# Kernel tuning notes

Measured on AMD Instinct MI355X. Metric: run time of the kernel, lower is better.

The kernel has to match this reference:

```python
import jax, jax.numpy as jnp
import numpy as np

K = 20
EPS = 1e-5
DIMS = [(8, 64), (64, 64), (64, 128), (128, 256), (256, 512), (512, 1024)]
EMB = 512


def edge_conv(x, W, gamma, beta):
    # x: [B, C, N]; W: [O, 2C]
    xt = jnp.swapaxes(x, 1, 2)                      # [B, N, C]
    inner = -2.0 * jnp.einsum('bnc,bmc->bnm', xt, xt)
    xx = jnp.sum(xt * xt, axis=-1)                  # [B, N]
    pd = -xx[:, :, None] - inner - xx[:, None, :]   # -||xi-xj||^2
    idx = jax.lax.top_k(pd, K)[1]                   # [B, N, K]
    nbr = jax.vmap(lambda f, i: f[i])(xt, idx)      # [B, N, K, C] gather
    ctr = xt[:, :, None, :]
    edge = jnp.concatenate([nbr - ctr, jnp.broadcast_to(ctr, nbr.shape)], axis=-1)  # [B,N,K,2C]
    h = jnp.einsum('bnkc,oc->bnko', edge, W)        # 1x1 conv
    mean = jnp.mean(h, axis=(0, 1, 2))
    var = jnp.var(h, axis=(0, 1, 2))
    h = (h - mean) * jax.lax.rsqrt(var + EPS) * gamma + beta  # BatchNorm2d (train stats)
    h = jnp.where(h > 0, h, 0.2 * h)                # LeakyReLU(0.2)
    return jnp.transpose(jnp.max(h, axis=2), (0, 2, 1))  # max over k -> [B, O, N]


def setup_inputs() -> dict:
    key = jax.random.key(0)
    ks = jax.random.split(key, 32)
    d = {"x": jax.random.normal(ks[0], (4, 8, 1024), dtype=jnp.float32)}
    for i, (cin, cout) in enumerate(DIMS):
        fan_in = 2 * cin
        std = float(np.sqrt(2.0 / ((1.0 + 0.2 ** 2) * fan_in)))
        d[f"W{i+1}"] = jax.random.normal(ks[1 + i], (cout, 2 * cin), dtype=jnp.float32) * std
        d[f"g{i+1}"] = jnp.ones((cout,), dtype=jnp.float32)
        d[f"b{i+1}"] = jnp.zeros((cout,), dtype=jnp.float32)
    d["Wm"] = jax.random.normal(ks[20], (EMB, 4096), dtype=jnp.float32) * float(1.0 / np.sqrt(4096))
    d["bm"] = jnp.zeros((EMB,), dtype=jnp.float32)
    d["gm"] = jnp.ones((EMB,), dtype=jnp.float32)
    d["betam"] = jnp.zeros((EMB,), dtype=jnp.float32)
    return d


def reference(x, W1, g1, b1, W2, g2, b2, W3, g3, b3, W4, g4, b4,
              W5, g5, b5, W6, g6, b6, Wm, bm, gm, betam):
    x1 = edge_conv(x, W1, g1, b1)
    x2 = edge_conv(x1, W2, g2, b2)
    x3 = edge_conv(x2, W3, g3, b3)
    x4 = edge_conv(x3, W4, g4, b4)
    x5 = edge_conv(x4, W5, g5, b5)
    x6 = edge_conv(x5, W6, g6, b6)
    feat = jnp.concatenate([x1, x2, x3, x4, x5, x6], axis=1)  # [B, 2048, N]
    p1 = jnp.max(feat, axis=-1)
    p2 = jnp.mean(feat, axis=-1)
    z = jnp.concatenate([p1, p2], axis=1) @ Wm.T + bm         # [B, 4096] -> [B, EMB]
    mean = jnp.mean(z, axis=0)
    var = jnp.var(z, axis=0)
    z = (z - mean) * jax.lax.rsqrt(var + EPS) * gm + betam    # BatchNorm1d
    return jnp.where(z > 0, z, 0.2 * z)
```

## Files before the change

kernel.cpp:

```cpp
#include <hip/hip_runtime.h>
#include <math.h>

#define BATCH 4
#define NPTS 1024
#define KNN 20
#define EPS 1e-5f
#define FEATC 2048


#define KC 16
__global__ __launch_bounds__(256, 2)
void gram_kernel(const float* __restrict__ x, int Cin, size_t bstride,
                 float* __restrict__ G) {
    int b = blockIdx.z;
    int n0 = blockIdx.y * 64;
    int m0 = blockIdx.x * 128;
    const float* xb = x + (size_t)b * bstride;
    __shared__ float As[KC][64];
    __shared__ float Bs[KC][128];
    int tid = threadIdx.x;
    int tn = tid % 16, tm = tid / 16;
    float acc[4][8] = {};

    const int ia = tid * 4, cca = ia >> 6, nna = ia & 63;
    const int ib = tid * 8, ccb = ib >> 7, mmb = ib & 127;
    float4 pa, pb0, pb1;
    auto prefetch = [&](int c0) {
        pa = make_float4(0.f, 0.f, 0.f, 0.f);
        pb0 = make_float4(0.f, 0.f, 0.f, 0.f);
        pb1 = make_float4(0.f, 0.f, 0.f, 0.f);
        if (c0 + cca < Cin) pa = *(const float4*)(xb + (size_t)(c0 + cca) * NPTS + n0 + nna);
        if (c0 + ccb < Cin) {
            const float* r = xb + (size_t)(c0 + ccb) * NPTS + m0 + mmb;
            pb0 = *(const float4*)(r);
            pb1 = *(const float4*)(r + 4);
        }
    };
    prefetch(0);
    for (int c0 = 0; c0 < Cin; c0 += KC) {
        *(float4*)(&As[cca][nna]) = pa;
        *(float4*)(&Bs[ccb][mmb]) = pb0;
        *(float4*)(&Bs[ccb][mmb + 4]) = pb1;
        __syncthreads();
        if (c0 + KC < Cin) prefetch(c0 + KC);
#pragma unroll
        for (int cc = 0; cc < KC; ++cc) {
            float4 a4 = *(const float4*)(&As[cc][tn * 4]);
            float4 b0 = *(const float4*)(&Bs[cc][tm * 8]);
            float4 b1 = *(const float4*)(&Bs[cc][tm * 8 + 4]);
            float a[4] = {a4.x, a4.y, a4.z, a4.w};
            float bb[8] = {b0.x, b0.y, b0.z, b0.w, b1.x, b1.y, b1.z, b1.w};
#pragma unroll
            for (int i = 0; i < 4; i++)
#pragma unroll
                for (int j = 0; j < 8; j++) acc[i][j] += a[i] * bb[j];
        }
        __syncthreads();
    }
    float* Gb = G + (size_t)b * NPTS * NPTS;
#pragma unroll
    for (int i = 0; i < 4; i++) {
        size_t row = (size_t)(n0 + tn * 4 + i) * NPTS + m0 + tm * 8;
        *(float4*)(Gb + row)     = make_float4(acc[i][0], acc[i][1], acc[i][2], acc[i][3]);
        *(float4*)(Gb + row + 4) = make_float4(acc[i][4], acc[i][5], acc[i][6], acc[i][7]);
    }
}

__global__ void diag_kernel(const float* __restrict__ G, float* __restrict__ xx) {
    int t = blockIdx.x * 256 + threadIdx.x;
    int b = t >> 10, n = t & (NPTS - 1);
    xx[t] = G[((size_t)b << 20) + (size_t)n * (NPTS + 1)];
}

__global__ __launch_bounds__(256)
void topk_kernel(const float* __restrict__ G, const float* __restrict__ xx,
                 int* __restrict__ idx) {
    int wid = threadIdx.x >> 6, lane = threadIdx.x & 63;
    int t = blockIdx.x * 4 + wid;
    int b = t >> 10, n = t & (NPTS - 1);
    const float* Gr = G + ((size_t)b * NPTS + n) * NPTS;
    const float* xxb = xx + b * NPTS;
    float xxn = xxb[n];
    float d[16];
    int base = lane * 4;
#pragma unroll
    for (int c = 0; c < 4; ++c) {
        float4 gv = *(const float4*)(Gr + c * 256 + base);
        float4 xv = *(const float4*)(xxb + c * 256 + base);
        d[c * 4 + 0] = (2.f * gv.x - xxn) - xv.x;
        d[c * 4 + 1] = (2.f * gv.y - xxn) - xv.y;
        d[c * 4 + 2] = (2.f * gv.z - xxn) - xv.z;
        d[c * 4 + 3] = (2.f * gv.w - xxn) - xv.w;
    }
    int* out = idx + (size_t)t * KNN;
    for (int k = 0; k < KNN; ++k) {
        float bv = d[0]; int bs = 0;
#pragma unroll
        for (int s = 1; s < 16; ++s)
            if (d[s] > bv) { bv = d[s]; bs = s; }
        int bm = ((bs >> 2) << 8) + base + (bs & 3);
#pragma unroll
        for (int off = 32; off >= 1; off >>= 1) {
            float ov = __shfl_xor(bv, off);
            int om = __shfl_xor(bm, off);
            if (ov > bv || (ov == bv && om < bm)) { bv = ov; bm = om; }
        }
        if (lane == 0) out[k] = bm;
        int rel = bm - base;
#pragma unroll
        for (int s = 0; s < 16; ++s)
            if (rel == (((s >> 2) << 8) | (s & 3))) d[s] = -INFINITY;
    }
}

__global__ __launch_bounds__(256, 2)
void pq_gemm_kernel(const float* __restrict__ x, int Cin, size_t bstride,
                    const float* __restrict__ W, int Cout,
                    float* __restrict__ p, float* __restrict__ q) {
    int b = blockIdx.z;
    int o0 = blockIdx.x * 64;
    int n0 = blockIdx.y * 64;
    const float* xb = x + (size_t)b * bstride;
    __shared__ float W1s[KC][64];
    __shared__ float WQs[KC][64];
    __shared__ float Xs[KC][64];
    int tid = threadIdx.x;
    int tn = tid % 16;
    int tm = tid / 16;
    float accp[4][4] = {};
    float accq[4][4] = {};

    const int ix = tid * 4, ccx = ix >> 6, nnx = ix & 63;
    const int r = tid % 64, cg = (tid / 64) * 4;
    const float* Wr = W + (size_t)(o0 + r) * 2 * Cin;
    float4 px, pw1, pw2;
    auto prefetch = [&](int c0) {
        px = make_float4(0.f, 0.f, 0.f, 0.f);
        pw1 = make_float4(0.f, 0.f, 0.f, 0.f);
        pw2 = make_float4(0.f, 0.f, 0.f, 0.f);
        if (c0 + ccx < Cin) px = *(const float4*)(xb + (size_t)(c0 + ccx) * NPTS + n0 + nnx);
        if (c0 + cg < Cin) {
            pw1 = *(const float4*)(Wr + c0 + cg);
            pw2 = *(const float4*)(Wr + Cin + c0 + cg);
        }
    };
    prefetch(0);
    for (int c0 = 0; c0 < Cin; c0 += KC) {
        *(float4*)(&Xs[ccx][nnx]) = px;
        W1s[cg + 0][r] = pw1.x; WQs[cg + 0][r] = pw2.x - pw1.x;
        W1s[cg + 1][r] = pw1.y; WQs[cg + 1][r] = pw2.y - pw1.y;
        W1s[cg + 2][r] = pw1.z; WQs[cg + 2][r] = pw2.z - pw1.z;
        W1s[cg + 3][r] = pw1.w; WQs[cg + 3][r] = pw2.w - pw1.w;
        __syncthreads();
        if (c0 + KC < Cin) prefetch(c0 + KC);
#pragma unroll
        for (int cc = 0; cc < KC; ++cc) {
            float4 wv = *(const float4*)(&W1s[cc][tn * 4]);
            float4 qv = *(const float4*)(&WQs[cc][tn * 4]);
            float4 xv = *(const float4*)(&Xs[cc][tm * 4]);
            float w1[4] = {wv.x, wv.y, wv.z, wv.w};
            float wq[4] = {qv.x, qv.y, qv.z, qv.w};
            float xj[4] = {xv.x, xv.y, xv.z, xv.w};
#pragma unroll
            for (int i = 0; i < 4; i++)
#pragma unroll
                for (int j = 0; j < 4; j++) {
                    accp[i][j] += w1[i] * xj[j];
                    accq[i][j] += wq[i] * xj[j];
                }
        }
        __syncthreads();
    }
#pragma unroll
    for (int j = 0; j < 4; j++) {
        int n = n0 + tm * 4 + j;
        size_t base = ((size_t)b * NPTS + n) * Cout + o0 + tn * 4;
        *(float4*)(p + base) = make_float4(accp[0][j], accp[1][j], accp[2][j], accp[3][j]);
        *(float4*)(q + base) = make_float4(accq[0][j], accq[1][j], accq[2][j], accq[3][j]);
    }
}

template <int COUT>
__global__ void stats_kernel(const float* __restrict__ p, const float* __restrict__ q,
                             const int* __restrict__ idx,
                             float* __restrict__ partials) {
    constexpr int CA = (COUT < 256) ? COUT : 256;
    constexpr int PP = 256 / CA;
    constexpr int NCH = COUT / CA;
    constexpr int NCHUNK = 16;
    int bid = blockIdx.x;
    int b = bid / (NPTS / NCHUNK);
    int n0 = (bid % (NPTS / NCHUNK)) * NCHUNK;
    int cl = threadIdx.x % CA;
    int c = blockIdx.y * CA + cl;
    int sub = threadIdx.x / CA;
    float s = 0.f, ss = 0.f;
    for (int nl = sub; nl < NCHUNK; nl += PP) {
        int n = n0 + nl;
        size_t nb = (size_t)b * NPTS + n;
        const int* ix = idx + nb * KNN;
        float qv = q[nb * COUT + c];
        for (int k = 0; k < KNN; ++k) {
            int m = ix[k];
            float v = p[((size_t)b * NPTS + m) * COUT + c] + qv;
            s += v;
            ss += v * v;
        }
    }
    __shared__ float red[256];
    float* outp = partials + ((size_t)bid * NCH + blockIdx.y) * 2 * CA;
    red[threadIdx.x] = s;
    __syncthreads();
    for (int st = PP / 2; st > 0; st >>= 1) {
        if (sub < st) red[threadIdx.x] += red[threadIdx.x + st * CA];
        __syncthreads();
    }
    if (sub == 0) outp[cl] = red[cl];
    __syncthreads();
    red[threadIdx.x] = ss;
    __syncthreads();
    for (int st = PP / 2; st > 0; st >>= 1) {
        if (sub < st) red[threadIdx.x] += red[threadIdx.x + st * CA];
        __syncthreads();
    }
    if (sub == 0) outp[CA + cl] = red[cl];
}

__global__ void scaleshift_kernel(const float* __restrict__ partials, const float* __restrict__ g,
                                  const float* __restrict__ beta, int Cout, int nblk,
                                  int CA, int NCH, float* __restrict__ sc) {
    int c = blockIdx.x * 256 + threadIdx.x;
    if (c >= Cout) return;
    int chunk = c / CA, within = c % CA;
    float s0 = 0.f, s1 = 0.f;
    for (int b = 0; b < nblk; ++b) {
        const float* pp = partials + ((size_t)b * NCH + chunk) * 2 * CA;
        s0 += pp[within];
        s1 += pp[CA + within];
    }
    float cnt = (float)(BATCH * NPTS * KNN);
    float mean = s0 / cnt;
    float var = s1 / cnt - mean * mean;
    float s = g[c] * rsqrtf(var + EPS);
    sc[c] = s;
    sc[Cout + c] = beta[c] - mean * s;
}

__global__ void apply_kernel(const float* __restrict__ p, const float* __restrict__ q,
                             const int* __restrict__ idx, const float* __restrict__ sc,
                             int Cout, int choff, float* __restrict__ feat) {
    __shared__ float tile[32][33];
    __shared__ int nidx[32][KNN];
    int b = blockIdx.z;
    int c0 = blockIdx.x * 32, n0 = blockIdx.y * 32;
    int tx = threadIdx.x % 32, ty = threadIdx.x / 32;
    for (int i = threadIdx.x; i < 32 * KNN; i += 256) {
        int nn = i / KNN, kk = i % KNN;
        nidx[nn][kk] = idx[((size_t)b * NPTS + n0 + nn) * KNN + kk];
    }
    __syncthreads();
    int c = c0 + tx;
    float s = sc[c], sh = sc[Cout + c];
    for (int i = ty; i < 32; i += 8) {
        int n = n0 + i;
        size_t nb = (size_t)b * NPTS + n;
        float qv = q[nb * Cout + c];
        float mx = -INFINITY, mn = INFINITY;
        for (int k = 0; k < KNN; ++k) {
            int m = nidx[i][k];
            float v = p[((size_t)b * NPTS + m) * Cout + c] + qv;
            mx = fmaxf(mx, v);
            mn = fminf(mn, v);
        }
        float v = (s >= 0.f) ? mx : mn;
        v = s * v + sh;
        tile[i][tx] = (v > 0.f) ? v : 0.2f * v;
    }
    __syncthreads();
    for (int i = ty; i < 32; i += 8) {
        feat[((size_t)b * FEATC + choff + c0 + i) * NPTS + n0 + tx] = tile[tx][i];
    }
}

__global__ void pool_kernel(const float* __restrict__ feat, float* __restrict__ pooled) {
    int t = blockIdx.x;
    int b = t >> 11, c = t & (FEATC - 1);
    const float* row = feat + (size_t)t * NPTS;
    int tid = threadIdx.x;
    float mx = -INFINITY, sm = 0.f;
    for (int n = tid; n < NPTS; n += 256) { float v = row[n]; mx = fmaxf(mx, v); sm += v; }
    __shared__ float smx[256], ssm[256];
    smx[tid] = mx; ssm[tid] = sm;
    __syncthreads();
    for (int s = 128; s > 0; s >>= 1) {
        if (tid < s) { smx[tid] = fmaxf(smx[tid], smx[tid + s]); ssm[tid] += ssm[tid + s]; }
        __syncthreads();
    }
    if (tid == 0) {
        pooled[b * 4096 + c] = smx[0];
        pooled[b * 4096 + 2048 + c] = ssm[0] * (1.f / NPTS);
    }
}

__global__ void final_kernel(const float* __restrict__ pooled, const float* __restrict__ Wm,
                             const float* __restrict__ bm, const float* __restrict__ gm,
                             const float* __restrict__ betam, float* __restrict__ out) {
    int o = blockIdx.x;
    int tid = threadIdx.x;
    float acc[BATCH] = {};
    for (int t = tid; t < 4096; t += 256) {
        float w = Wm[(size_t)o * 4096 + t];
#pragma unroll
        for (int b = 0; b < BATCH; b++) acc[b] += w * pooled[b * 4096 + t];
    }
    __shared__ float red[256];
    float zb[BATCH];
    for (int b = 0; b < BATCH; b++) {
        red[tid] = acc[b];
        __syncthreads();
        for (int s = 128; s > 0; s >>= 1) {
            if (tid < s) red[tid] += red[tid + s];
            __syncthreads();
        }
        zb[b] = red[0];
        __syncthreads();
    }
    if (tid == 0) {
        float z[BATCH];
        float mean = 0.f;
        for (int b = 0; b < BATCH; b++) { z[b] = zb[b] + bm[o]; mean += z[b]; }
        mean *= (1.f / BATCH);
        float var = 0.f;
        for (int b = 0; b < BATCH; b++) { float d = z[b] - mean; var += d * d; }
        var *= (1.f / BATCH);
        float s = gm[o] * rsqrtf(var + EPS);
        for (int b = 0; b < BATCH; b++) {
            float v = (z[b] - mean) * s + betam[o];
            out[b * 512 + o] = (v > 0.f) ? v : 0.2f * v;
        }
    }
}

extern "C" void kernel_launch(void* const* d_in, const int* in_sizes, int n_in,
                              void* d_out, int out_size, void* d_ws, size_t ws_size,
                              hipStream_t stream) {
    const float* x = (const float*)d_in[0];
    const float* Wm = (const float*)d_in[19];
    const float* bm = (const float*)d_in[20];
    const float* gm = (const float*)d_in[21];
    const float* betam = (const float*)d_in[22];
    float* out = (float*)d_out;

    char* ws = (char*)d_ws;
    float* G        = (float*)(ws);
    float* p        = G;
    float* q        = (float*)(ws + (size_t)(16 << 20));
    float* feat     = (float*)(ws + (size_t)(32 << 20));
    int*   idx      = (int*)  (ws + (size_t)(64 << 20));
    float* xx       = (float*)(ws + (size_t)(64 << 20) + (384 << 10));
    float* sc       = (float*)(ws + (size_t)(64 << 20) + (448 << 10));
    float* pooled   = (float*)(ws + (size_t)(64 << 20) + (512 << 10));
    float* partials = (float*)(ws + (size_t)(65 << 20));

    const int cins[6]   = {8, 64, 64, 128, 256, 512};
    const int couts[6]  = {64, 64, 128, 256, 512, 1024};
    const int choffs[6] = {0, 64, 128, 256, 512, 1024};

    const float* xin = x;
    size_t bstride = (size_t)8 * NPTS;
    const int NBLK = BATCH * (NPTS / 16);

    for (int L = 0; L < 6; ++L) {
        int Cin = cins[L], Cout = couts[L], choff = choffs[L];
        const float* W = (const float*)d_in[1 + 3 * L];
        const float* g = (const float*)d_in[2 + 3 * L];
        const float* bb = (const float*)d_in[3 + 3 * L];

        gram_kernel<<<dim3(NPTS / 128, NPTS / 64, BATCH), 256, 0, stream>>>(xin, Cin, bstride, G);
        diag_kernel<<<BATCH * NPTS / 256, 256, 0, stream>>>(G, xx);
        topk_kernel<<<BATCH * NPTS / 4, 256, 0, stream>>>(G, xx, idx);
        pq_gemm_kernel<<<dim3(Cout / 64, NPTS / 64, BATCH), 256, 0, stream>>>(xin, Cin, bstride, W, Cout, p, q);
        int CA = (Cout < 256) ? Cout : 256;
        int NCH = Cout / CA;
        switch (Cout) {
            case 64:   stats_kernel<64>  <<<dim3(NBLK, 1), 256, 0, stream>>>(p, q, idx, partials); break;
            case 128:  stats_kernel<128> <<<dim3(NBLK, 1), 256, 0, stream>>>(p, q, idx, partials); break;
            case 256:  stats_kernel<256> <<<dim3(NBLK, 1), 256, 0, stream>>>(p, q, idx, partials); break;
            case 512:  stats_kernel<512> <<<dim3(NBLK, 2), 256, 0, stream>>>(p, q, idx, partials); break;
            case 1024: stats_kernel<1024><<<dim3(NBLK, 4), 256, 0, stream>>>(p, q, idx, partials); break;
        }
        scaleshift_kernel<<<(Cout + 255) / 256, 256, 0, stream>>>(partials, g, bb, Cout, NBLK, CA, NCH, sc);
        apply_kernel<<<dim3(Cout / 32, NPTS / 32, BATCH), 256, 0, stream>>>(p, q, idx, sc, Cout, choff, feat);

        xin = feat + (size_t)choff * NPTS;
        bstride = (size_t)FEATC * NPTS;
    }

    pool_kernel<<<BATCH * FEATC, 256, 0, stream>>>(feat, pooled);
    final_kernel<<<512, 256, 0, stream>>>(pooled, Wm, bm, gm, betam, out);
}
```

Measured before the change: 1.159 ms.

## Add 128x128-tile Gram and PQ GEMM kernels and fuse diagonal extraction

Adds larger 128x128 register-tiled variants of the Gram-matrix and point/weight GEMM kernels, used for the deeper layers (Cin>=256, Cout>=1024). Each thread now computes an 8x8 tile, which raises arithmetic intensity and cuts shared-memory traffic per FMA. The squared-norm diagonal is written straight from the Gram accumulators, so the separate diag kernel launch goes away. The cost is more registers per thread (the PQ variant holds two 8x8 accumulators), fewer blocks per GEMM, and lower occupancy.

```diff
diff --git a/kernel.cpp b/kernel.cpp
--- a/kernel.cpp
+++ b/kernel.cpp
@@ -6,12 +6,12 @@
 #define KNN 20
 #define EPS 1e-5f
 #define FEATC 2048
-
-
 #define KC 16
+
+
 __global__ __launch_bounds__(256, 2)
 void gram_kernel(const float* __restrict__ x, int Cin, size_t bstride,
-                 float* __restrict__ G) {
+                 float* __restrict__ G, float* __restrict__ xx) {
     int b = blockIdx.z;
     int n0 = blockIdx.y * 64;
     int m0 = blockIdx.x * 128;
@@ -60,16 +60,75 @@
     float* Gb = G + (size_t)b * NPTS * NPTS;
 #pragma unroll
     for (int i = 0; i < 4; i++) {
-        size_t row = (size_t)(n0 + tn * 4 + i) * NPTS + m0 + tm * 8;
+        int n = n0 + tn * 4 + i;
+        size_t row = (size_t)n * NPTS + m0 + tm * 8;
         *(float4*)(Gb + row)     = make_float4(acc[i][0], acc[i][1], acc[i][2], acc[i][3]);
         *(float4*)(Gb + row + 4) = make_float4(acc[i][4], acc[i][5], acc[i][6], acc[i][7]);
-    }
-}
-
-__global__ void diag_kernel(const float* __restrict__ G, float* __restrict__ xx) {
-    int t = blockIdx.x * 256 + threadIdx.x;
-    int b = t >> 10, n = t & (NPTS - 1);
-    xx[t] = G[((size_t)b << 20) + (size_t)n * (NPTS + 1)];
+#pragma unroll
+        for (int j = 0; j < 8; j++)
+            if (n == m0 + tm * 8 + j) xx[b * NPTS + n] = acc[i][j];
+    }
+}
+
+__global__ __launch_bounds__(256, 2)
+void gram128_kernel(const float* __restrict__ x, int Cin, size_t bstride,
+                    float* __restrict__ G, float* __restrict__ xx) {
+    int b = blockIdx.z;
+    int n0 = blockIdx.y * 128;
+    int m0 = blockIdx.x * 128;
+    const float* xb = x + (size_t)b * bstride;
+    __shared__ float As[KC][128];
+    __shared__ float Bs[KC][128];
+    int tid = threadIdx.x;
+    int tn = tid % 16, tm = tid / 16;
+    float acc[8][8] = {};
+
+    const int cca = tid / 16, nna = (tid * 8) & 127;
+    float4 pa0, pa1, pb0, pb1;
+    auto prefetch = [&](int c0) {
+        const float* ra = xb + (size_t)(c0 + cca) * NPTS + n0 + nna;
+        const float* rb = xb + (size_t)(c0 + cca) * NPTS + m0 + nna;
+        pa0 = *(const float4*)(ra);
+        pa1 = *(const float4*)(ra + 4);
+        pb0 = *(const float4*)(rb);
+        pb1 = *(const float4*)(rb + 4);
+    };
+    prefetch(0);
+    for (int c0 = 0; c0 < Cin; c0 += KC) {
+        *(float4*)(&As[cca][nna]) = pa0;
+        *(float4*)(&As[cca][nna + 4]) = pa1;
+        *(float4*)(&Bs[cca][nna]) = pb0;
+        *(float4*)(&Bs[cca][nna + 4]) = pb1;
+        __syncthreads();
+        if (c0 + KC < Cin) prefetch(c0 + KC);
+#pragma unroll
+        for (int cc = 0; cc < KC; ++cc) {
+            float4 a0 = *(const float4*)(&As[cc][tn * 4]);
+            float4 a1 = *(const float4*)(&As[cc][64 + tn * 4]);
+            float4 b0 = *(const float4*)(&Bs[cc][tm * 4]);
+            float4 b1 = *(const float4*)(&Bs[cc][64 + tm * 4]);
+            float a[8] = {a0.x, a0.y, a0.z, a0.w, a1.x, a1.y, a1.z, a1.w};
+            float bb[8] = {b0.x, b0.y, b0.z, b0.w, b1.x, b1.y, b1.z, b1.w};
+#pragma unroll
+            for (int i = 0; i < 8; i++)
+#pragma unroll
+                for (int j = 0; j < 8; j++) acc[i][j] += a[i] * bb[j];
+        }
+        __syncthreads();
+    }
+    float* Gb = G + (size_t)b * NPTS * NPTS;
+#pragma unroll
+    for (int i = 0; i < 8; i++) {
+        int n = n0 + (i < 4 ? tn * 4 + i : 64 + tn * 4 + (i - 4));
+        size_t row = (size_t)n * NPTS;
+        *(float4*)(Gb + row + m0 + tm * 4)      = make_float4(acc[i][0], acc[i][1], acc[i][2], acc[i][3]);
+        *(float4*)(Gb + row + m0 + 64 + tm * 4) = make_float4(acc[i][4], acc[i][5], acc[i][6], acc[i][7]);
+#pragma unroll
+        for (int j = 0; j < 8; j++) {
+            int m = m0 + (j < 4 ? tm * 4 + j : 64 + tm * 4 + (j - 4));
+            if (n == m) xx[b * NPTS + n] = acc[i][j];
+        }
+    }
 }
 
 __global__ __launch_bounds__(256)
@@ -177,6 +236,82 @@
         size_t base = ((size_t)b * NPTS + n) * Cout + o0 + tn * 4;
         *(float4*)(p + base) = make_float4(accp[0][j], accp[1][j], accp[2][j], accp[3][j]);
         *(float4*)(q + base) = make_float4(accq[0][j], accq[1][j], accq[2][j], accq[3][j]);
+    }
+}
+
+__global__ __launch_bounds__(256, 2)
+void pq128_kernel(const float* __restrict__ x, int Cin, size_t bstride,
+                  const float* __restrict__ W, int Cout,
+                  float* __restrict__ p, float* __restrict__ q) {
+    int b = blockIdx.z;
+    int o0 = blockIdx.x * 128;
+    int n0 = blockIdx.y * 128;
+    const float* xb = x + (size_t)b * bstride;
+    __shared__ float W1s[KC][128];
+    __shared__ float WQs[KC][128];
+    __shared__ float Xs[KC][128];
+    int tid = threadIdx.x;
+    int tn = tid % 16;
+    int tm = tid / 16;
+    float accp[8][8] = {};
+    float accq[8][8] = {};
+
+    const int ccx = tid / 16, nnx = (tid * 8) & 127;
+    const int r = tid % 128, cg = (tid / 128) * 8;
+    const float* Wr = W + (size_t)(o0 + r) * 2 * Cin;
+    float4 px0, px1, pw1a, pw1b, pw2a, pw2b;
+    auto prefetch = [&](int c0) {
+        const float* rx = xb + (size_t)(c0 + ccx) * NPTS + n0 + nnx;
+        px0 = *(const float4*)(rx);
+        px1 = *(const float4*)(rx + 4);
+        pw1a = *(const float4*)(Wr + c0 + cg);
+        pw1b = *(const float4*)(Wr + c0 + cg + 4);
+        pw2a = *(const float4*)(Wr + Cin + c0 + cg);
+        pw2b = *(const float4*)(Wr + Cin + c0 + cg + 4);
+    };
+    prefetch(0);
+    for (int c0 = 0; c0 < Cin; c0 += KC) {
+        *(float4*)(&Xs[ccx][nnx]) = px0;
+        *(float4*)(&Xs[ccx][nnx + 4]) = px1;
+        W1s[cg + 0][r] = pw1a.x; WQs[cg + 0][r] = pw2a.x - pw1a.x;
+        W1s[cg + 1][r] = pw1a.y; WQs[cg + 1][r] = pw2a.y - pw1a.y;
+        W1s[cg + 2][r] = pw1a.z; WQs[cg + 2][r] = pw2a.z - pw1a.z;
+        W1s[cg + 3][r] = pw1a.w; WQs[cg + 3][r] = pw2a.w - pw1a.w;
+        W1s[cg + 4][r] = pw1b.x; WQs[cg + 4][r] = pw2b.x - pw1b.x;
+        W1s[cg + 5][r] = pw1b.y; WQs[cg + 5][r] = pw2b.y - pw1b.y;
+        W1s[cg + 6][r] = pw1b.z; WQs[cg + 6][r] = pw2b.z - pw1b.z;
+        W1s[cg + 7][r] = pw1b.w; WQs[cg + 7][r] = pw2b.w - pw1b.w;
+        __syncthreads();
+        if (c0 + KC < Cin) prefetch(c0 + KC);
+#pragma unroll
+        for (int cc = 0; cc < KC; ++cc) {
+            float4 w0 = *(const float4*)(&W1s[cc][tn * 4]);
+            float4 w1v = *(const float4*)(&W1s[cc][64 + tn * 4]);
+            float4 q0 = *(const float4*)(&WQs[cc][tn * 4]);
+            float4 q1 = *(const float4*)(&WQs[cc][64 + tn * 4]);
+            float4 x0 = *(const float4*)(&Xs[cc][tm * 4]);
+            float4 x1 = *(const float4*)(&Xs[cc][64 + tm * 4]);
+            float w1[8] = {w0.x, w0.y, w0.z, w0.w, w1v.x, w1v.y, w1v.z, w1v.w};
+            float wq[8] = {q0.x, q0.y, q0.z, q0.w, q1.x, q1.y, q1.z, q1.w};
+            float xj[8] = {x0.x, x0.y, x0.z, x0.w, x1.x, x1.y, x1.z, x1.w};
+#pragma unroll
+            for (int i = 0; i < 8; i++)
+#pragma unroll
+                for (int j = 0; j < 8; j++) {
+                    accp[i][j] += w1[i] * xj[j];
+                    accq[i][j] += wq[i] * xj[j];
+                }
+        }
+        __syncthreads();
+    }
+#pragma unroll
+    for (int j = 0; j < 8; j++) {
+        int n = n0 + (j < 4 ? tm * 4 + j : 64 + tm * 4 + (j - 4));
+        size_t base = ((size_t)b * NPTS + n) * Cout + o0;
+        *(float4*)(p + base + tn * 4)      = make_float4(accp[0][j], accp[1][j], accp[2][j], accp[3][j]);
+        *(float4*)(p + base + 64 + tn * 4) = make_float4(accp[4][j], accp[5][j], accp[6][j], accp[7][j]);
+        *(float4*)(q + base + tn * 4)      = make_float4(accq[0][j], accq[1][j], accq[2][j], accq[3][j]);
+        *(float4*)(q + base + 64 + tn * 4) = make_float4(accq[4][j], accq[5][j], accq[6][j], accq[7][j]);
     }
 }
 
@@ -376,10 +511,15 @@
         const float* g = (const float*)d_in[2 + 3 * L];
         const float* bb = (const float*)d_in[3 + 3 * L];
 
-        gram_kernel<<<dim3(NPTS / 128, NPTS / 64, BATCH), 256, 0, stream>>>(xin, Cin, bstride, G);
-        diag_kernel<<<BATCH * NPTS / 256, 256, 0, stream>>>(G, xx);
+        if (Cin >= 256)
+            gram128_kernel<<<dim3(NPTS / 128, NPTS / 128, BATCH), 256, 0, stream>>>(xin, Cin, bstride, G, xx);
+        else
+            gram_kernel<<<dim3(NPTS / 128, NPTS / 64, BATCH), 256, 0, stream>>>(xin, Cin, bstride, G, xx);
         topk_kernel<<<BATCH * NPTS / 4, 256, 0, stream>>>(G, xx, idx);
-        pq_gemm_kernel<<<dim3(Cout / 64, NPTS / 64, BATCH), 256, 0, stream>>>(xin, Cin, bstride, W, Cout, p, q);
+        if (Cout >= 1024)
+            pq128_kernel<<<dim3(Cout / 128, NPTS / 128, BATCH), 256, 0, stream>>>(xin, Cin, bstride, W, Cout, p, q);
+        else
+            pq_gemm_kernel<<<dim3(Cout / 64, NPTS / 64, BATCH), 256, 0, stream>>>(xin, Cin, bstride, W, Cout, p, q);
         int CA = (Cout < 256) ? Cout : 256;
         int NCH = Cout / CA;
         switch (Cout) {
```

Measured after the change: 1.305 ms. +12.6%, slower.
